# Optimization experiments

Measured on AMD Instinct MI355X. Metric: run time of the kernel, lower is better.

The kernel has to match this reference:

```python
import jax, jax.numpy as jnp
import numpy as np
import math

E = 16          # num_experts
TOP_K = 2       # num_experts_per_tok (used as capacity_factor in EC routing)
D = 1024        # embed_dim
F = 4096        # expert_hidden_dim = mlp_ratio * D
SH = 2048       # shared intermediate = F * n_shared_experts // mlp_ratio


def setup_inputs() -> dict:
    key = jax.random.key(0)
    ks = jax.random.split(key, 10)
    s = lambda k, shape, fan: jax.random.normal(k, shape, jnp.float32) / np.sqrt(fan)
    return {
        "x": jax.random.normal(ks[0], (32, 256, D), jnp.float32),
        "gate_w": s(ks[1], (E, D), D),                 # ECMoEGate.weight
        "up_w": s(ks[2], (E, F, D), D),                # fused_up.weight
        "up_b": s(ks[3], (E, F), D),                   # fused_up.bias
        "gw": s(ks[4], (E, F, D), D),                  # fused_gate.weight
        "gb": s(ks[5], (E, F), D),                     # fused_gate.bias
        "down_w": s(ks[6], (E, D, F), F),              # fused_down.weight
        "down_b": s(ks[7], (E, D), F),                 # fused_down.bias
        "sh_gate_w": s(ks[8], (SH, D), D),             # shared_experts.gate_proj
        "sh_up_w": s(ks[9], (SH, D), D),               # shared_experts.up_proj
        "sh_down_w": s(jax.random.fold_in(key, 11), (D, SH), SH),  # shared_experts.down_proj
    }


def reference(x, gate_w, up_w, up_b, gw, gb, down_w, down_b, sh_gate_w, sh_up_w, sh_down_w):
    B, S, Dm = x.shape
    h = x.reshape(-1, Dm)                               # [T, D]
    T = h.shape[0]
    # gate: sigmoid scores, expert-choice top-k over tokens per expert
    scores = jax.nn.sigmoid(h @ gate_w.T)               # [T, E]
    cap = math.ceil(T / E * TOP_K)                      # capacity per expert
    topk_score, topk_ids = jax.lax.top_k(scores.T, cap) # [E, cap]
    # dispatch: gather tokens per expert
    xin = h[topk_ids]                                   # [E, cap, D]
    # batched expert GLU (baddbmm equivalent)
    up = jnp.einsum('ecd,efd->ecf', xin, up_w) + up_b[:, None, :]
    g = jnp.einsum('ecd,efd->ecf', xin, gw) + gb[:, None, :]
    eo = jax.nn.silu(g) * up                            # [E, cap, F]
    eo = jnp.einsum('ecf,edf->ecd', eo, down_w) + down_b[:, None, :]
    # combine: weighted scatter-add back to token positions
    flat = (eo * topk_score[..., None]).reshape(-1, Dm) # [E*cap, D]
    out = jnp.zeros_like(h).at[topk_ids.reshape(-1)].add(flat)
    out = out.reshape(B, S, Dm)
    # shared dense GLU MLP (SiLU)
    shared = (jax.nn.silu(jnp.einsum('bsd,fd->bsf', x, sh_gate_w))
              * jnp.einsum('bsd,fd->bsf', x, sh_up_w))
    shared = jnp.einsum('bsf,df->bsd', shared, sh_down_w)
    return out + shared
```

## Files before the change

### kernel.cpp

```cpp
#include <hip/hip_runtime.h>
#include <hip/hip_bf16.h>

#define Tn 8192
#define Dn 1024
#define Fn 4096
#define SHn 2048
#define En 16
#define CAPn 1024

typedef __bf16 bf16_t;
typedef bf16_t bf16x8 __attribute__((ext_vector_type(8)));
typedef float f32x4 __attribute__((ext_vector_type(4)));
typedef float f32x16 __attribute__((ext_vector_type(16)));

__device__ __forceinline__ unsigned short f2bf(float f) {
  unsigned int u = __builtin_bit_cast(unsigned int, f);
  u += 0x7FFFu + ((u >> 16) & 1u);
  return (unsigned short)(u >> 16);
}
__device__ __forceinline__ unsigned int pack2(float a, float b) {
  return (unsigned int)f2bf(a) | ((unsigned int)f2bf(b) << 16);
}

__device__ __forceinline__ void gload16(const void* g, void* l) {
  __builtin_amdgcn_global_load_lds(
      (const __attribute__((address_space(1))) unsigned int*)g,
      (__attribute__((address_space(3))) unsigned int*)l, 16, 0, 0);
}

__global__ __launch_bounds__(256) void kcvt(const float* __restrict__ s,
                                            unsigned short* __restrict__ d, int n8) {
  int i = blockIdx.x * 256 + threadIdx.x;
  int stride = gridDim.x * 256;
  const float4* sv = (const float4*)s;
  for (; i < n8; i += stride) {
    float4 a = sv[2 * i], b = sv[2 * i + 1];
    uint4 u = { pack2(a.x, a.y), pack2(a.z, a.w), pack2(b.x, b.y), pack2(b.z, b.w) };
    ((uint4*)d)[i] = u;
  }
}

__global__ __launch_bounds__(256) void kscores(const float* __restrict__ x,
                                               const float* __restrict__ gw,
                                               float* __restrict__ sc) {
  __shared__ float sx[Dn];
  int tid = threadIdx.x, tok = blockIdx.x;
  ((float4*)sx)[tid] = ((const float4*)(x + (size_t)tok * Dn))[tid];
  __syncthreads();
  int e = tid >> 4, kl = tid & 15;
  const float4* w = (const float4*)(gw + e * Dn);
  const float4* xv = (const float4*)sx;
  float acc = 0.f;
#pragma unroll
  for (int j = 0; j < 16; ++j) {
    float4 a = w[kl + 16 * j], b = xv[kl + 16 * j];
    acc += a.x * b.x + a.y * b.y + a.z * b.z + a.w * b.w;
  }
#pragma unroll
  for (int off = 8; off; off >>= 1) acc += __shfl_xor(acc, off, 64);
  if (kl == 0) sc[(size_t)e * Tn + tok] = 1.f / (1.f + expf(-acc));
}

__global__ __launch_bounds__(256) void kselect(const float* __restrict__ scores,
                                               int* __restrict__ ids,
                                               float* __restrict__ oscore) {
  __shared__ unsigned int keys[Tn];
  __shared__ unsigned int hist[256];
  __shared__ unsigned int sh_prefix, sh_k, sh_cnt, sh_eq;
  __shared__ int eqlist[1024];
  const int tid = threadIdx.x, e = blockIdx.x;
  const float* row = scores + (size_t)e * Tn;
  for (int i = 0; i < Tn / 256; ++i)
    keys[tid + i * 256] = __float_as_uint(row[tid + i * 256]);
  if (tid == 0) { sh_prefix = 0u; sh_k = CAPn; }
  __syncthreads();
  for (int shift = 24; shift >= 0; shift -= 8) {
    hist[tid] = 0u;
    __syncthreads();
    unsigned int prefix = sh_prefix;
    unsigned int mask = (shift == 24) ? 0u : (0xFFFFFFFFu << (shift + 8));
    for (int i = 0; i < Tn / 256; ++i) {
      unsigned int kk = keys[tid + i * 256];
      if ((kk & mask) == prefix) atomicAdd(&hist[(kk >> shift) & 255], 1u);
    }
    __syncthreads();
    if (tid == 0) {
      unsigned int k = sh_k, c = 0; int b;
      for (b = 255; b >= 0; --b) { c += hist[b]; if (c >= k) break; }
      sh_k = k - (c - hist[b]);
      sh_prefix = prefix | ((unsigned int)b << shift);
    }
    __syncthreads();
  }
  const unsigned int thr = sh_prefix;
  if (tid == 0) { sh_cnt = 0u; sh_eq = 0u; }
  __syncthreads();
  const int base = e * CAPn;
  for (int i = 0; i < Tn / 256; ++i) {
    int t = tid + i * 256;
    unsigned int kk = keys[t];
    if (kk > thr) {
      unsigned int p = atomicAdd(&sh_cnt, 1u);
      ids[base + p] = t;
      oscore[base + p] = __uint_as_float(kk);
    } else if (kk == thr) {
      unsigned int p = atomicAdd(&sh_eq, 1u);
      if (p < 1024u) eqlist[p] = t;
    }
  }
  __syncthreads();
  if (tid == 0) {
    int need = CAPn - (int)sh_cnt;
    int m = (int)sh_eq; if (m > 1024) m = 1024;
    for (int j = 0; j < need; ++j) {
      int best = 1 << 30, bi = 0;
      for (int i2 = 0; i2 < m; ++i2)
        if (eqlist[i2] < best) { best = eqlist[i2]; bi = i2; }
      eqlist[bi] = 1 << 30;
      ids[base + (int)sh_cnt + j] = best;
      oscore[base + (int)sh_cnt + j] = __uint_as_float(thr);
    }
  }
}


template <bool GATHER>
__global__ __launch_bounds__(256, 2) void kglu_bf(
    const unsigned short* __restrict__ X, const int* __restrict__ idsg,
    const unsigned short* __restrict__ Wg, const unsigned short* __restrict__ Wu,
    const float* __restrict__ biasg, const float* __restrict__ biasu,
    unsigned short* __restrict__ H, int N, int Mz, int MB, int NB) {
  constexpr int K = Dn;
  __shared__ alignas(16) unsigned char sA[16384];
  __shared__ alignas(16) unsigned char sB1[16384];
  __shared__ alignas(16) unsigned char sB2[16384];
  __shared__ int sIds[128];
  const int tid = threadIdx.x;
  const int nwg = gridDim.x;
  const int cpx = nwg >> 3;
  const int bid = blockIdx.x;
  const int swz = (bid & 7) * cpx + (bid >> 3);
  const int bm = swz % MB;
  const int bn = (swz / MB) % NB;
  const int z  = swz / (MB * NB);
  const int lane = tid & 63, w = tid >> 6;
  const int wm = w >> 1, wn = w & 1;
  const int row32 = lane & 31, kh = lane >> 5;
  const int row0 = bm * 128;

  if (tid < 128) sIds[tid] = GATHER ? idsg[z * CAPn + row0 + tid] : (row0 + tid);
  __syncthreads();

  const int lr = lane >> 3;
  const int lc = lane & 7;
  const int srcb = ((lc ^ lr) << 4);
  const unsigned char* Xb = (const unsigned char*)X;
  const unsigned char* Gb = (const unsigned char*)Wg + (size_t)z * N * (K * 2);
  const unsigned char* Ub = (const unsigned char*)Wu + (size_t)z * N * (K * 2);
  const unsigned char* aP[4];
#pragma unroll
  for (int i = 0; i < 4; ++i) {
    int ar = w * 32 + 8 * i + lr;
    aP[i] = Xb + (size_t)sIds[ar] * (K * 2) + srcb;
  }
  const int br0 = bn * 128 + w * 32 + lr;
  const unsigned char* gP0 = Gb + (size_t)br0 * (K * 2) + srcb;
  const unsigned char* uP0 = Ub + (size_t)br0 * (K * 2) + srcb;

  f32x16 accG[2][2], accU[2][2];
#pragma unroll
  for (int m = 0; m < 2; ++m)
#pragma unroll
    for (int n = 0; n < 2; ++n) {
      accG[m][n] = (f32x16)(0.f);
      accU[m][n] = (f32x16)(0.f);
    }

  for (int k0b = 0; k0b < K * 2; k0b += 128) {
    __syncthreads();
#pragma unroll
    for (int i = 0; i < 4; ++i) {
      unsigned ldsoff = (unsigned)(w * 32 + 8 * i) * 128u;
      gload16(aP[i] + k0b, sA + ldsoff);
      gload16(gP0 + (size_t)i * 8 * (K * 2) + k0b, sB1 + ldsoff);
      gload16(uP0 + (size_t)i * 8 * (K * 2) + k0b, sB2 + ldsoff);
    }
    __syncthreads();
#pragma unroll
    for (int ks = 0; ks < 4; ++ks) {
      const int swb = (((ks * 2 + kh) ^ (row32 & 7)) << 4);
      bf16x8 av[2], gv[2], uv[2];
#pragma unroll
      for (int m = 0; m < 2; ++m)
        av[m] = *(const bf16x8*)(sA + (wm * 64 + m * 32 + row32) * 128 + swb);
#pragma unroll
      for (int n = 0; n < 2; ++n) {
        gv[n] = *(const bf16x8*)(sB1 + (wn * 64 + n * 32 + row32) * 128 + swb);
        uv[n] = *(const bf16x8*)(sB2 + (wn * 64 + n * 32 + row32) * 128 + swb);
      }
#pragma unroll
      for (int m = 0; m < 2; ++m)
#pragma unroll
        for (int n = 0; n < 2; ++n) {
          accG[m][n] = __builtin_amdgcn_mfma_f32_32x32x16_bf16(av[m], gv[n], accG[m][n], 0, 0, 0);
          accU[m][n] = __builtin_amdgcn_mfma_f32_32x32x16_bf16(av[m], uv[n], accU[m][n], 0, 0, 0);
        }
    }
  }
#pragma unroll
  for (int n = 0; n < 2; ++n) {
    int col = bn * 128 + wn * 64 + n * 32 + row32;
    float bg = biasg ? biasg[(size_t)z * N + col] : 0.f;
    float bu = biasu ? biasu[(size_t)z * N + col] : 0.f;
#pragma unroll
    for (int m = 0; m < 2; ++m) {
#pragma unroll
      for (int reg = 0; reg < 16; ++reg) {
        float g = accG[m][n][reg] + bg;
        float u = accU[m][n][reg] + bu;
        float h = g / (1.f + __expf(-g)) * u;
        int row = row0 + wm * 64 + m * 32 + (reg & 3) + 8 * (reg >> 2) + 4 * kh;
        H[(size_t)z * Mz * N + (size_t)row * N + col] = f2bf(h);
      }
    }
  }
}

template <int K, bool SCATTER>
__global__ __launch_bounds__(256, 2) void kdown_bf(
    const unsigned short* __restrict__ Hin, const unsigned short* __restrict__ W,
    const float* __restrict__ bias, const int* __restrict__ idsg,
    const float* __restrict__ scg, float* __restrict__ Out, int Mz, int MB, int NB) {
  constexpr int N = Dn;
  __shared__ alignas(16) unsigned char sA[16384];
  __shared__ alignas(16) unsigned char sB[16384];
  __shared__ int sIds[128];
  __shared__ float sSc[128];
  const int tid = threadIdx.x;
  const int nwg = gridDim.x;
  const int cpx = nwg >> 3;
  const int bid = blockIdx.x;
  const int swz = (bid & 7) * cpx + (bid >> 3);
  const int bm = swz % MB;
  const int bn = (swz / MB) % NB;
  const int z  = swz / (MB * NB);
  const int lane = tid & 63, w = tid >> 6;
  const int wm = w >> 1, wn = w & 1;
  const int row32 = lane & 31, kh = lane >> 5;
  const int row0 = bm * 128;

  if (SCATTER && tid < 128) {
    sIds[tid] = idsg[z * CAPn + row0 + tid];
    sSc[tid] = scg[z * CAPn + row0 + tid];
  }
  __syncthreads();

  const int lr = lane >> 3;
  const int lc = lane & 7;
  const int srcb = ((lc ^ lr) << 4);
  const unsigned char* Ab = (const unsigned char*)Hin + (size_t)z * Mz * (K * 2);
  const unsigned char* Wb = (const unsigned char*)W + (size_t)z * N * (K * 2);
  const int ar0 = row0 + w * 32 + lr;
  const int br0 = bn * 128 + w * 32 + lr;
  const unsigned char* aP0 = Ab + (size_t)ar0 * (K * 2) + srcb;
  const unsigned char* bP0 = Wb + (size_t)br0 * (K * 2) + srcb;

  f32x16 acc[2][2];
#pragma unroll
  for (int m = 0; m < 2; ++m)
#pragma unroll
    for (int n = 0; n < 2; ++n) acc[m][n] = (f32x16)(0.f);

  for (int k0b = 0; k0b < K * 2; k0b += 128) {
    __syncthreads();
#pragma unroll
    for (int i = 0; i < 4; ++i) {
      unsigned ldsoff = (unsigned)(w * 32 + 8 * i) * 128u;
      gload16(aP0 + (size_t)i * 8 * (K * 2) + k0b, sA + ldsoff);
      gload16(bP0 + (size_t)i * 8 * (K * 2) + k0b, sB + ldsoff);
    }
    __syncthreads();
#pragma unroll
    for (int ks = 0; ks < 4; ++ks) {
      const int swb = (((ks * 2 + kh) ^ (row32 & 7)) << 4);
      bf16x8 av[2], bv[2];
#pragma unroll
      for (int m = 0; m < 2; ++m)
        av[m] = *(const bf16x8*)(sA + (wm * 64 + m * 32 + row32) * 128 + swb);
#pragma unroll
      for (int n = 0; n < 2; ++n)
        bv[n] = *(const bf16x8*)(sB + (wn * 64 + n * 32 + row32) * 128 + swb);
#pragma unroll
      for (int m = 0; m < 2; ++m)
#pragma unroll
        for (int n = 0; n < 2; ++n)
          acc[m][n] = __builtin_amdgcn_mfma_f32_32x32x16_bf16(av[m], bv[n], acc[m][n], 0, 0, 0);
    }
  }
#pragma unroll
  for (int n = 0; n < 2; ++n) {
    int col = bn * 128 + wn * 64 + n * 32 + row32;
    float bvv = bias ? bias[(size_t)z * N + col] : 0.f;
#pragma unroll
    for (int m = 0; m < 2; ++m) {
#pragma unroll
      for (int reg = 0; reg < 16; ++reg) {
        int rl = wm * 64 + m * 32 + (reg & 3) + 8 * (reg >> 2) + 4 * kh;
        float v = acc[m][n][reg] + bvv;
        if (SCATTER) {
          atomicAdd(Out + (size_t)sIds[rl] * Dn + col, sSc[rl] * v);
        } else {
          Out[(size_t)(row0 + rl) * Dn + col] = v;
        }
      }
    }
  }
}

extern "C" void kernel_launch(void* const* d_in, const int* in_sizes, int n_in,
                              void* d_out, int out_size, void* d_ws, size_t ws_size,
                              hipStream_t stream) {
  const float* x      = (const float*)d_in[0];
  const float* gate_w = (const float*)d_in[1];
  const float* up_w   = (const float*)d_in[2];
  const float* up_b   = (const float*)d_in[3];
  const float* gw     = (const float*)d_in[4];
  const float* gb     = (const float*)d_in[5];
  const float* down_w = (const float*)d_in[6];
  const float* down_b = (const float*)d_in[7];
  const float* shg    = (const float*)d_in[8];
  const float* shu    = (const float*)d_in[9];
  const float* shd    = (const float*)d_in[10];
  float* out = (float*)d_out;

  const size_t H_BYTES  = (size_t)En * CAPn * Fn * 2;
  const size_t XB_BYTES = (size_t)Tn * Dn * 2;
  const size_t WE_BYTES = (size_t)En * Fn * Dn * 2;
  const size_t SH_BYTES = (size_t)SHn * Dn * 2;
  const size_t SC_BYTES = (size_t)En * Tn * 4;
  const size_t ID_BYTES = (size_t)En * CAPn * 4;
  const size_t need = H_BYTES + XB_BYTES + 3 * WE_BYTES + 3 * SH_BYTES +
                      SC_BYTES + 2 * ID_BYTES;
  if (ws_size < need) return;

  char* p = (char*)d_ws;
  unsigned short* H    = (unsigned short*)p; p += H_BYTES;
  unsigned short* xb   = (unsigned short*)p; p += XB_BYTES;
  unsigned short* upb  = (unsigned short*)p; p += WE_BYTES;
  unsigned short* gwb  = (unsigned short*)p; p += WE_BYTES;
  unsigned short* dwb  = (unsigned short*)p; p += WE_BYTES;
  unsigned short* shgb = (unsigned short*)p; p += SH_BYTES;
  unsigned short* shub = (unsigned short*)p; p += SH_BYTES;
  unsigned short* shdb = (unsigned short*)p; p += SH_BYTES;
  float* scores = (float*)p; p += SC_BYTES;
  int* ids      = (int*)p;  p += ID_BYTES;
  float* osc    = (float*)p;

  kcvt<<<2048, 256, 0, stream>>>(x, xb, Tn * Dn / 8);
  kscores<<<Tn, 256, 0, stream>>>(x, gate_w, scores);
  kselect<<<En, 256, 0, stream>>>(scores, ids, osc);
  kcvt<<<2048, 256, 0, stream>>>(up_w, upb, En * Fn * Dn / 8);
  kcvt<<<2048, 256, 0, stream>>>(gw, gwb, En * Fn * Dn / 8);
  kcvt<<<2048, 256, 0, stream>>>(down_w, dwb, En * Dn * Fn / 8);
  kcvt<<<256, 256, 0, stream>>>(shg, shgb, SHn * Dn / 8);
  kcvt<<<256, 256, 0, stream>>>(shu, shub, SHn * Dn / 8);
  kcvt<<<256, 256, 0, stream>>>(shd, shdb, Dn * SHn / 8);

  kglu_bf<false><<<(Tn / 128) * (SHn / 128), 256, 0, stream>>>(
      xb, nullptr, shgb, shub, nullptr, nullptr, H, SHn, Tn, Tn / 128, SHn / 128);
  kdown_bf<SHn, false><<<(Tn / 128) * (Dn / 128), 256, 0, stream>>>(
      H, shdb, nullptr, nullptr, nullptr, out, Tn, Tn / 128, Dn / 128);

  kglu_bf<true><<<(CAPn / 128) * (Fn / 128) * En, 256, 0, stream>>>(
      xb, ids, gwb, upb, gb, up_b, H, Fn, CAPn, CAPn / 128, Fn / 128);
  kdown_bf<Fn, true><<<(CAPn / 128) * (Dn / 128) * En, 256, 0, stream>>>(
      H, dwb, down_b, ids, osc, out, CAPn, CAPn / 128, Dn / 128);
}
```

Before: 997.3 us.

## Fuse weight conversions into GEMM launches and switch to 16x16x32 MFMA

The separate fp32-to-bf16 conversion kernels are removed. The x conversion and the shared-weight conversions now run inside the scores kernel, and the expert weight conversions run as extra blocks appended to the preceding GLU GEMM launches, so conversion overlaps with GEMM work and launch overhead drops. All GEMMs also move from 32x32x16 MFMA tiles to 16x16x32 tiles with a 4x4 accumulator layout. The appended conversion blocks compete with the GEMM blocks for CUs, and the new MFMA shape changes how LDS reads and registers are used.

```diff
diff --git a/kernel.cpp b/kernel.cpp
--- a/kernel.cpp
+++ b/kernel.cpp
@@ -11,7 +11,6 @@
 typedef __bf16 bf16_t;
 typedef bf16_t bf16x8 __attribute__((ext_vector_type(8)));
 typedef float f32x4 __attribute__((ext_vector_type(4)));
-typedef float f32x16 __attribute__((ext_vector_type(16)));
 
 __device__ __forceinline__ unsigned short f2bf(float f) {
   unsigned int u = __builtin_bit_cast(unsigned int, f);
@@ -28,24 +27,38 @@
       (__attribute__((address_space(3))) unsigned int*)l, 16, 0, 0);
 }
 
-__global__ __launch_bounds__(256) void kcvt(const float* __restrict__ s,
-                                            unsigned short* __restrict__ d, int n8) {
-  int i = blockIdx.x * 256 + threadIdx.x;
-  int stride = gridDim.x * 256;
-  const float4* sv = (const float4*)s;
-  for (; i < n8; i += stride) {
-    float4 a = sv[2 * i], b = sv[2 * i + 1];
-    uint4 u = { pack2(a.x, a.y), pack2(a.z, a.w), pack2(b.x, b.y), pack2(b.z, b.w) };
-    ((uint4*)d)[i] = u;
-  }
-}
-
-__global__ __launch_bounds__(256) void kscores(const float* __restrict__ x,
-                                               const float* __restrict__ gw,
-                                               float* __restrict__ sc) {
+__device__ __forceinline__ void conv_blocks(int cb, int ncb, int tid,
+                                            const float* s1, unsigned short* d1, int n1,
+                                            const float* s2, unsigned short* d2, int n2) {
+  const int tot = n1 + n2;
+  for (int i = cb * 256 + tid; i < tot; i += ncb * 256) {
+    const float4* sv; uint4* dv; int j;
+    if (i < n1) { j = i; sv = (const float4*)s1; dv = (uint4*)d1; }
+    else        { j = i - n1; sv = (const float4*)s2; dv = (uint4*)d2; }
+    float4 a = sv[2 * j], b = sv[2 * j + 1];
+    dv[j] = uint4{ pack2(a.x, a.y), pack2(a.z, a.w), pack2(b.x, b.y), pack2(b.z, b.w) };
+  }
+}
+
+__global__ __launch_bounds__(256) void kscores_cvt(
+    const float* __restrict__ x, const float* __restrict__ gw,
+    float* __restrict__ sc, unsigned short* __restrict__ xb,
+    const float* __restrict__ shg, unsigned short* __restrict__ shgb,
+    const float* __restrict__ shu, unsigned short* __restrict__ shub,
+    const float* __restrict__ shd, unsigned short* __restrict__ shdb) {
   __shared__ float sx[Dn];
-  int tid = threadIdx.x, tok = blockIdx.x;
-  ((float4*)sx)[tid] = ((const float4*)(x + (size_t)tok * Dn))[tid];
+  const int tid = threadIdx.x;
+  if (blockIdx.x >= Tn) {
+    const int cb = blockIdx.x - Tn, ncb = gridDim.x - Tn;
+    constexpr int nsh = SHn * Dn / 8;
+    conv_blocks(cb, ncb, tid, shg, shgb, nsh, shu, shub, nsh);
+    conv_blocks(cb, ncb, tid, shd, shdb, nsh, nullptr, nullptr, 0);
+    return;
+  }
+  const int tok = blockIdx.x;
+  float4 v = ((const float4*)(x + (size_t)tok * Dn))[tid];
+  ((float4*)sx)[tid] = v;
+  ((uint2*)(xb + (size_t)tok * Dn))[tid] = uint2{ pack2(v.x, v.y), pack2(v.z, v.w) };
   __syncthreads();
   int e = tid >> 4, kl = tid & 15;
   const float4* w = (const float4*)(gw + e * Dn);
@@ -129,23 +142,29 @@
     const unsigned short* __restrict__ X, const int* __restrict__ idsg,
     const unsigned short* __restrict__ Wg, const unsigned short* __restrict__ Wu,
     const float* __restrict__ biasg, const float* __restrict__ biasu,
-    unsigned short* __restrict__ H, int N, int Mz, int MB, int NB) {
+    unsigned short* __restrict__ H, int N, int Mz, int MB, int NB,
+    int gemmN,
+    const float* __restrict__ cS1, unsigned short* __restrict__ cD1, int cn1,
+    const float* __restrict__ cS2, unsigned short* __restrict__ cD2, int cn2) {
   constexpr int K = Dn;
   __shared__ alignas(16) unsigned char sA[16384];
   __shared__ alignas(16) unsigned char sB1[16384];
   __shared__ alignas(16) unsigned char sB2[16384];
   __shared__ int sIds[128];
   const int tid = threadIdx.x;
-  const int nwg = gridDim.x;
-  const int cpx = nwg >> 3;
   const int bid = blockIdx.x;
+  if (bid >= gemmN) {
+    conv_blocks(bid - gemmN, gridDim.x - gemmN, tid, cS1, cD1, cn1, cS2, cD2, cn2);
+    return;
+  }
+  const int cpx = gemmN >> 3;
   const int swz = (bid & 7) * cpx + (bid >> 3);
   const int bm = swz % MB;
   const int bn = (swz / MB) % NB;
   const int z  = swz / (MB * NB);
   const int lane = tid & 63, w = tid >> 6;
   const int wm = w >> 1, wn = w & 1;
-  const int row32 = lane & 31, kh = lane >> 5;
+  const int lrow = lane & 15, lk = lane >> 4;
   const int row0 = bm * 128;
 
   if (tid < 128) sIds[tid] = GATHER ? idsg[z * CAPn + row0 + tid] : (row0 + tid);
@@ -167,13 +186,13 @@
   const unsigned char* gP0 = Gb + (size_t)br0 * (K * 2) + srcb;
   const unsigned char* uP0 = Ub + (size_t)br0 * (K * 2) + srcb;
 
-  f32x16 accG[2][2], accU[2][2];
-#pragma unroll
-  for (int m = 0; m < 2; ++m)
-#pragma unroll
-    for (int n = 0; n < 2; ++n) {
-      accG[m][n] = (f32x16)(0.f);
-      accU[m][n] = (f32x16)(0.f);
+  f32x4 accG[4][4], accU[4][4];
+#pragma unroll
+  for (int m = 0; m < 4; ++m)
+#pragma unroll
+    for (int n = 0; n < 4; ++n) {
+      accG[m][n] = {0.f, 0.f, 0.f, 0.f};
+      accU[m][n] = {0.f, 0.f, 0.f, 0.f};
     }
 
   for (int k0b = 0; k0b < K * 2; k0b += 128) {
@@ -187,39 +206,39 @@
     }
     __syncthreads();
 #pragma unroll
-    for (int ks = 0; ks < 4; ++ks) {
-      const int swb = (((ks * 2 + kh) ^ (row32 & 7)) << 4);
-      bf16x8 av[2], gv[2], uv[2];
-#pragma unroll
-      for (int m = 0; m < 2; ++m)
-        av[m] = *(const bf16x8*)(sA + (wm * 64 + m * 32 + row32) * 128 + swb);
-#pragma unroll
-      for (int n = 0; n < 2; ++n) {
-        gv[n] = *(const bf16x8*)(sB1 + (wn * 64 + n * 32 + row32) * 128 + swb);
-        uv[n] = *(const bf16x8*)(sB2 + (wn * 64 + n * 32 + row32) * 128 + swb);
+    for (int ks = 0; ks < 2; ++ks) {
+      const int swb = (((ks * 4 + lk) ^ (lrow & 7)) << 4);
+      bf16x8 av[4], gv[4], uv[4];
+#pragma unroll
+      for (int m = 0; m < 4; ++m)
+        av[m] = *(const bf16x8*)(sA + (wm * 64 + m * 16 + lrow) * 128 + swb);
+#pragma unroll
+      for (int n = 0; n < 4; ++n) {
+        gv[n] = *(const bf16x8*)(sB1 + (wn * 64 + n * 16 + lrow) * 128 + swb);
+        uv[n] = *(const bf16x8*)(sB2 + (wn * 64 + n * 16 + lrow) * 128 + swb);
       }
 #pragma unroll
-      for (int m = 0; m < 2; ++m)
-#pragma unroll
-        for (int n = 0; n < 2; ++n) {
-          accG[m][n] = __builtin_amdgcn_mfma_f32_32x32x16_bf16(av[m], gv[n], accG[m][n], 0, 0, 0);
-          accU[m][n] = __builtin_amdgcn_mfma_f32_32x32x16_bf16(av[m], uv[n], accU[m][n], 0, 0, 0);
+      for (int m = 0; m < 4; ++m)
+#pragma unroll
+        for (int n = 0; n < 4; ++n) {
+          accG[m][n] = __builtin_amdgcn_mfma_f32_16x16x32_bf16(av[m], gv[n], accG[m][n], 0, 0, 0);
+          accU[m][n] = __builtin_amdgcn_mfma_f32_16x16x32_bf16(av[m], uv[n], accU[m][n], 0, 0, 0);
         }
     }
   }
 #pragma unroll
-  for (int n = 0; n < 2; ++n) {
-    int col = bn * 128 + wn * 64 + n * 32 + row32;
+  for (int n = 0; n < 4; ++n) {
+    int col = bn * 128 + wn * 64 + n * 16 + lrow;
     float bg = biasg ? biasg[(size_t)z * N + col] : 0.f;
     float bu = biasu ? biasu[(size_t)z * N + col] : 0.f;
 #pragma unroll
-    for (int m = 0; m < 2; ++m) {
-#pragma unroll
-      for (int reg = 0; reg < 16; ++reg) {
-        float g = accG[m][n][reg] + bg;
-        float u = accU[m][n][reg] + bu;
+    for (int m = 0; m < 4; ++m) {
+#pragma unroll
+      for (int j = 0; j < 4; ++j) {
+        float g = accG[m][n][j] + bg;
+        float u = accU[m][n][j] + bu;
         float h = g / (1.f + __expf(-g)) * u;
-        int row = row0 + wm * 64 + m * 32 + (reg & 3) + 8 * (reg >> 2) + 4 * kh;
+        int row = row0 + wm * 64 + m * 16 + lk * 4 + j;
         H[(size_t)z * Mz * N + (size_t)row * N + col] = f2bf(h);
       }
     }
@@ -246,7 +265,7 @@
   const int z  = swz / (MB * NB);
   const int lane = tid & 63, w = tid >> 6;
   const int wm = w >> 1, wn = w & 1;
-  const int row32 = lane & 31, kh = lane >> 5;
+  const int lrow = lane & 15, lk = lane >> 4;
   const int row0 = bm * 128;
 
   if (SCATTER && tid < 128) {
@@ -265,11 +284,11 @@
   const unsigned char* aP0 = Ab + (size_t)ar0 * (K * 2) + srcb;
   const unsigned char* bP0 = Wb + (size_t)br0 * (K * 2) + srcb;
 
-  f32x16 acc[2][2];
-#pragma unroll
-  for (int m = 0; m < 2; ++m)
-#pragma unroll
-    for (int n = 0; n < 2; ++n) acc[m][n] = (f32x16)(0.f);
+  f32x4 acc[4][4];
+#pragma unroll
+  for (int m = 0; m < 4; ++m)
+#pragma unroll
+    for (int n = 0; n < 4; ++n) acc[m][n] = {0.f, 0.f, 0.f, 0.f};
 
   for (int k0b = 0; k0b < K * 2; k0b += 128) {
     __syncthreads();
@@ -281,32 +300,32 @@
     }
     __syncthreads();
 #pragma unroll
-    for (int ks = 0; ks < 4; ++ks) {
-      const int swb = (((ks * 2 + kh) ^ (row32 & 7)) << 4);
-      bf16x8 av[2], bv[2];
-#pragma unroll
-      for (int m = 0; m < 2; ++m)
-        av[m] = *(const bf16x8*)(sA + (wm * 64 + m * 32 + row32) * 128 + swb);
-#pragma unroll
-      for (int n = 0; n < 2; ++n)
-        bv[n] = *(const bf16x8*)(sB + (wn * 64 + n * 32 + row32) * 128 + swb);
-#pragma unroll
-      for (int m = 0; m < 2; ++m)
-#pragma unroll
-        for (int n = 0; n < 2; ++n)
-          acc[m][n] = __builtin_amdgcn_mfma_f32_32x32x16_bf16(av[m], bv[n], acc[m][n], 0, 0, 0);
-    }
-  }
-#pragma unroll
-  for (int n = 0; n < 2; ++n) {
-    int col = bn * 128 + wn * 64 + n * 32 + row32;
+    for (int ks = 0; ks < 2; ++ks) {
+      const int swb = (((ks * 4 + lk) ^ (lrow & 7)) << 4);
+      bf16x8 av[4], bv[4];
+#pragma unroll
+      for (int m = 0; m < 4; ++m)
+        av[m] = *(const bf16x8*)(sA + (wm * 64 + m * 16 + lrow) * 128 + swb);
+#pragma unroll
+      for (int n = 0; n < 4; ++n)
+        bv[n] = *(const bf16x8*)(sB + (wn * 64 + n * 16 + lrow) * 128 + swb);
+#pragma unroll
+      for (int m = 0; m < 4; ++m)
+#pragma unroll
+        for (int n = 0; n < 4; ++n)
+          acc[m][n] = __builtin_amdgcn_mfma_f32_16x16x32_bf16(av[m], bv[n], acc[m][n], 0, 0, 0);
+    }
+  }
+#pragma unroll
+  for (int n = 0; n < 4; ++n) {
+    int col = bn * 128 + wn * 64 + n * 16 + lrow;
     float bvv = bias ? bias[(size_t)z * N + col] : 0.f;
 #pragma unroll
-    for (int m = 0; m < 2; ++m) {
-#pragma unroll
-      for (int reg = 0; reg < 16; ++reg) {
-        int rl = wm * 64 + m * 32 + (reg & 3) + 8 * (reg >> 2) + 4 * kh;
-        float v = acc[m][n][reg] + bvv;
+    for (int m = 0; m < 4; ++m) {
+#pragma unroll
+      for (int j = 0; j < 4; ++j) {
+        int rl = wm * 64 + m * 16 + lk * 4 + j;
+        float v = acc[m][n][j] + bvv;
         if (SCATTER) {
           atomicAdd(Out + (size_t)sIds[rl] * Dn + col, sSc[rl] * v);
         } else {
@@ -356,23 +375,23 @@
   int* ids      = (int*)p;  p += ID_BYTES;
   float* osc    = (float*)p;
 
-  kcvt<<<2048, 256, 0, stream>>>(x, xb, Tn * Dn / 8);
-  kscores<<<Tn, 256, 0, stream>>>(x, gate_w, scores);
+  constexpr int NWE8 = En * Fn * Dn / 8;
+
+  kscores_cvt<<<Tn + 256, 256, 0, stream>>>(x, gate_w, scores, xb,
+                                            shg, shgb, shu, shub, shd, shdb);
   kselect<<<En, 256, 0, stream>>>(scores, ids, osc);
-  kcvt<<<2048, 256, 0, stream>>>(up_w, upb, En * Fn * Dn / 8);
-  kcvt<<<2048, 256, 0, stream>>>(gw, gwb, En * Fn * Dn / 8);
-  kcvt<<<2048, 256, 0, stream>>>(down_w, dwb, En * Dn * Fn / 8);
-  kcvt<<<256, 256, 0, stream>>>(shg, shgb, SHn * Dn / 8);
-  kcvt<<<256, 256, 0, stream>>>(shu, shub, SHn * Dn / 8);
-  kcvt<<<256, 256, 0, stream>>>(shd, shdb, Dn * SHn / 8);
-
-  kglu_bf<false><<<(Tn / 128) * (SHn / 128), 256, 0, stream>>>(
-      xb, nullptr, shgb, shub, nullptr, nullptr, H, SHn, Tn, Tn / 128, SHn / 128);
+
+  kglu_bf<false><<<(Tn / 128) * (SHn / 128) + 2048, 256, 0, stream>>>(
+      xb, nullptr, shgb, shub, nullptr, nullptr, H, SHn, Tn, Tn / 128, SHn / 128,
+      (Tn / 128) * (SHn / 128), up_w, upb, NWE8, gw, gwb, NWE8);
+
   kdown_bf<SHn, false><<<(Tn / 128) * (Dn / 128), 256, 0, stream>>>(
       H, shdb, nullptr, nullptr, nullptr, out, Tn, Tn / 128, Dn / 128);
 
-  kglu_bf<true><<<(CAPn / 128) * (Fn / 128) * En, 256, 0, stream>>>(
-      xb, ids, gwb, upb, gb, up_b, H, Fn, CAPn, CAPn / 128, Fn / 128);
+  kglu_bf<true><<<(CAPn / 128) * (Fn / 128) * En + 1024, 256, 0, stream>>>(
+      xb, ids, gwb, upb, gb, up_b, H, Fn, CAPn, CAPn / 128, Fn / 128,
+      (CAPn / 128) * (Fn / 128) * En, down_w, dwb, NWE8, nullptr, nullptr, 0);
+
   kdown_bf<Fn, true><<<(CAPn / 128) * (Dn / 128) * En, 256, 0, stream>>>(
       H, dwb, down_b, ids, osc, out, CAPn, CAPn / 128, Dn / 128);
 }
```

Result: faster. 967.3 us (-3.0%).
